# Optimization experiments

Hardware: AMD Instinct MI355X
Metric: run time of the kernel (lower is better)

Reference implementation:

```python
import jax, jax.numpy as jnp
import numpy as np

TEMPERATURE = 11.313708498984761  # sqrt(d_k) with d_k=128
RELU15_CAP = 15.0


def setup_inputs() -> dict:
    key = jax.random.key(0)
    kq, kk, kv = jax.random.split(key, 3)
    B, H, S, D = 4, 16, 1024, 128
    q = jax.random.normal(kq, (B, H, S, D), dtype=jnp.float32)
    k = jax.random.normal(kk, (B, H, S, D), dtype=jnp.float32)
    v = jax.random.normal(kv, (B, H, S, D), dtype=jnp.float32)
    mask = jnp.ones((B, 1, S, S), dtype=jnp.int32)  # broadcast over heads
    return {"q": q, "k": k, "v": v, "mask": mask}


def reference(q, k, v, mask):
    # attn = (q / temperature) @ k^T  -> [B,H,Sq,Sk]
    attn = jnp.einsum("bhqd,bhkd->bhqk", q / TEMPERATURE, k)
    # masked_fill(mask == 0, -1e9)
    attn = jnp.where(mask == 0, jnp.float32(-1e9), attn)
    # ReLU15 activation (custom softmax replacement): clamp to [0, 15]
    attn = jnp.clip(attn, 0.0, RELU15_CAP)
    # dropout with p=0.0 is identity (inference reference)
    out = jnp.einsum("bhqk,bhkd->bhqd", attn, v)
    return (out, attn)
```

## Files before the change

kernel.cpp:

```cpp
#include <hip/hip_runtime.h>
#include <stdint.h>

#define B_   4
#define H_   16
#define S_   1024
#define D_   128
#define BM   64
#define BN   32
#define NKT  (S_ / BN)
#define NTHREADS 256

typedef float f32x4 __attribute__((ext_vector_type(4)));
typedef short s16x8 __attribute__((ext_vector_type(8)));
typedef short s16x4 __attribute__((ext_vector_type(4)));

static __device__ __forceinline__ uint16_t f2bf(float f) {
  uint32_t u = __float_as_uint(f);
  u += 0x7FFFu + ((u >> 16) & 1u);
  return (uint16_t)(u >> 16);
}
static __device__ __forceinline__ float bf2f(uint16_t h) {
  return __uint_as_float((uint32_t)h << 16);
}

static __device__ __forceinline__ void gl16(const void* g, void* l) {
  __builtin_amdgcn_global_load_lds(
      (const __attribute__((address_space(1))) unsigned int*)g,
      (__attribute__((address_space(3))) unsigned int*)l, 16, 0, 0);
}

#define WSK_BYTES  16777216
#define WSV_BYTES  16777216
#define WSM_BYTES  524288
#define WS_NEED    (WSK_BYTES + WSV_BYTES + WSM_BYTES)

__global__ __launch_bounds__(256)
void prepass_kernel(const float* __restrict__ k, const float* __restrict__ v,
                    const int* __restrict__ mask,
                    char* __restrict__ wsK, char* __restrict__ wsV,
                    uint32_t* __restrict__ wsM)
{
  int gid = blockIdx.x * 256 + threadIdx.x;
  if (gid < 1048576) {
    int tile = gid >> 9, c = gid & 511;
    int ks = c >> 7, nt = (c >> 6) & 1, lane = c & 63;
    int row = (tile & 31) * 32 + 16 * nt + (lane & 15);
    int col = 32 * ks + 8 * (lane >> 4);
    const float* src = k + ((size_t)(tile >> 5) * S_ + row) * D_ + col;
    f32x4 x0 = *(const f32x4*)src;
    f32x4 x1 = *(const f32x4*)(src + 4);
    s16x8 h;
    h[0]=f2bf(x0[0]); h[1]=f2bf(x0[1]); h[2]=f2bf(x0[2]); h[3]=f2bf(x0[3]);
    h[4]=f2bf(x1[0]); h[5]=f2bf(x1[1]); h[6]=f2bf(x1[2]); h[7]=f2bf(x1[3]);
    *(s16x8*)(wsK + (size_t)gid * 16) = h;
  } else if (gid < 2097152) {
    int gv = gid - 1048576;
    int tile = gv >> 9, c = gv & 511;
    int nt = c >> 6, lane = c & 63;
    int d   = 16 * nt + (lane & 15);
    int kv0 = (tile & 31) * 32 + 8 * (lane >> 4);
    const float* src = v + ((size_t)(tile >> 5) * S_ + kv0) * D_ + d;
    s16x8 h;
    #pragma unroll
    for (int i = 0; i < 8; ++i) h[i] = f2bf(src[(size_t)i * D_]);
    *(s16x8*)(wsV + (size_t)gv * 16) = h;
  } else if (gid < 2228224) {
    int gm = gid - 2097152;
    const int* src = mask + (size_t)(gm >> 5) * S_ + (gm & 31) * 32;
    uint32_t bits = 0;
    #pragma unroll
    for (int i = 0; i < 32; ++i) bits |= (src[i] != 0 ? 1u : 0u) << i;
    wsM[gm] = bits;
  }
}

__global__ __launch_bounds__(NTHREADS)
__attribute__((amdgpu_waves_per_eu(4)))
void attn_relu15_main(const float* __restrict__ q,
                      const char* __restrict__ wsK, const char* __restrict__ wsV,
                      const uint32_t* __restrict__ wsM,
                      float* __restrict__ outp, float* __restrict__ attnp)
{
  const int blk = blockIdx.x;
  const int g   = (blk & 7) * 128 + (blk >> 3);
  const int bh  = g >> 4;
  const int qt  = g & 15;
  const int b   = bh >> 4;

  const int tid  = threadIdx.x;
  const int lane = tid & 63;
  const int wq   = tid >> 6;
  const int lhi  = lane >> 4;
  const int llo  = lane & 15;

  __shared__ __align__(16) char smem[36864];
  char* const lK0 = smem;
  char* const lV0 = smem + 16384;
  char* const lS  = smem + 32768 + wq * 1024;

  const float*    qg  = q + (size_t)bh * (S_ * D_) + (size_t)qt * BM * D_;
  const char*     kw  = wsK + (size_t)(bh * 32) * 8192;
  const char*     vw  = wsV + (size_t)(bh * 32) * 8192;
  const uint32_t* mw0 = wsM + (size_t)(b * 1024 + qt * BM + 16 * wq) * 32;
  float*          ag  = attnp + (size_t)bh * S_ * S_ + (size_t)qt * BM * S_;
  float*          og  = outp  + (size_t)bh * (S_ * D_) + (size_t)qt * BM * D_;

  const float invT = 0.08838834764831843f;

  s16x8 qf[4];
  {
    const float* qrow = qg + (size_t)(16 * wq + llo) * D_;
    #pragma unroll
    for (int ks = 0; ks < 4; ++ks) {
      int d0 = 32 * ks + 8 * lhi;
      f32x4 x0 = *(const f32x4*)(qrow + d0);
      f32x4 x1 = *(const f32x4*)(qrow + d0 + 4);
      s16x8 h;
      h[0]=f2bf(x0[0]*invT); h[1]=f2bf(x0[1]*invT); h[2]=f2bf(x0[2]*invT); h[3]=f2bf(x0[3]*invT);
      h[4]=f2bf(x1[0]*invT); h[5]=f2bf(x1[1]*invT); h[6]=f2bf(x1[2]*invT); h[7]=f2bf(x1[3]*invT);
      qf[ks] = h;
    }
  }

  #pragma unroll
  for (int rep = 0; rep < 2; ++rep) {
    gl16(kw + rep * 4096 + tid * 16, lK0 + rep * 4096 + wq * 1024);
    gl16(vw + rep * 4096 + tid * 16, lV0 + rep * 4096 + wq * 1024);
  }
  asm volatile("s_waitcnt vmcnt(0)" ::: "memory");
  __builtin_amdgcn_s_barrier();
  __builtin_amdgcn_sched_barrier(0);

  f32x4 oacc[8];
  #pragma unroll
  for (int i = 0; i < 8; ++i) oacc[i] = (f32x4){0.f,0.f,0.f,0.f};

  int cur = 0;
  for (int kt = 0; kt < NKT; ++kt) {
    const bool pf = (kt + 1 < NKT);
    char* lKc = lK0 + cur * 8192;
    char* lVc = lV0 + cur * 8192;

    uint32_t mwv[4];
    #pragma unroll
    for (int j = 0; j < 4; ++j)
      mwv[j] = mw0[(size_t)(4 * lhi + j) * 32 + kt];

    if (pf) {
      const char* kn = kw + (size_t)(kt + 1) * 8192;
      const char* vn = vw + (size_t)(kt + 1) * 8192;
      char* lKn = lK0 + (cur ^ 1) * 8192;
      char* lVn = lV0 + (cur ^ 1) * 8192;
      #pragma unroll
      for (int rep = 0; rep < 2; ++rep) {
        gl16(kn + rep * 4096 + tid * 16, lKn + rep * 4096 + wq * 1024);
        gl16(vn + rep * 4096 + tid * 16, lVn + rep * 4096 + wq * 1024);
      }
    }
    __builtin_amdgcn_sched_barrier(0);

    f32x4 sacc[2];
    sacc[0] = (f32x4){0.f,0.f,0.f,0.f}; sacc[1] = sacc[0];
    #pragma unroll
    for (int ks = 0; ks < 4; ++ks) {
      s16x8 bfr[2];
      #pragma unroll
      for (int nt = 0; nt < 2; ++nt)
        bfr[nt] = *(s16x8*)(lKc + (ks * 2 + nt) * 1024 + lane * 16);
      #pragma unroll
      for (int nt = 0; nt < 2; ++nt)
        sacc[nt] = __builtin_amdgcn_mfma_f32_16x16x32_bf16(qf[ks], bfr[nt], sacc[nt], 0, 0, 0);
    }

    #pragma unroll
    for (int nt = 0; nt < 2; ++nt) {
      char* sb = lS + (2 * nt + (llo >> 3)) * 256 + (llo & 7) * 2;
      #pragma unroll
      for (int j = 0; j < 4; ++j) {
        float val = fminf(fmaxf(sacc[nt][j], 0.f), 15.f);
        if (!((mwv[j] >> (16 * nt + llo)) & 1u)) val = 0.f;
        *(uint16_t*)(sb + (4 * lhi + j) * 16) = f2bf(val);
      }
    }

    {
      s16x8 saf = *(s16x8*)(lS + lane * 16);
      #pragma unroll
      for (int nt = 0; nt < 8; ++nt) {
        s16x8 vb = *(s16x8*)(lVc + nt * 1024 + lane * 16);
        oacc[nt] = __builtin_amdgcn_mfma_f32_16x16x32_bf16(saf, vb, oacc[nt], 0, 0, 0);
      }
    }

    #pragma unroll
    for (int p = 0; p < 2; ++p) {
      int r  = 16 * wq + p * 8 + (lane >> 3);
      int cb = lane & 7;
      s16x4 sv = *(s16x4*)(lS + (cb >> 1) * 256 + (((8 * p + (lane >> 3)) & 15) * 16) + (cb & 1) * 8);
      f32x4 a;
      a[0]=bf2f((uint16_t)sv[0]); a[1]=bf2f((uint16_t)sv[1]);
      a[2]=bf2f((uint16_t)sv[2]); a[3]=bf2f((uint16_t)sv[3]);
      __builtin_nontemporal_store(a, (f32x4*)(ag + (size_t)r * S_ + kt * BN + cb * 4));
    }

    asm volatile("s_waitcnt vmcnt(2)" ::: "memory");
    __builtin_amdgcn_s_barrier();
    __builtin_amdgcn_sched_barrier(0);
    cur ^= 1;
  }

  #pragma unroll
  for (int nt = 0; nt < 8; ++nt) {
    int n = 16 * nt + llo;
    #pragma unroll
    for (int j = 0; j < 4; ++j) {
      int m = 16 * wq + 4 * lhi + j;
      __builtin_nontemporal_store(oacc[nt][j], og + (size_t)m * D_ + n);
    }
  }
}

#define LDS_BARRIER() do {                                   \
    asm volatile("s_waitcnt lgkmcnt(0)" ::: "memory");       \
    __builtin_amdgcn_s_barrier();                            \
    __builtin_amdgcn_sched_barrier(0);                       \
  } while (0)

__global__ __launch_bounds__(NTHREADS)
__attribute__((amdgpu_waves_per_eu(4, 4)))
void attn_relu15_fallback(const float* __restrict__ q, const float* __restrict__ k,
                          const float* __restrict__ v, const int* __restrict__ mask,
                          float* __restrict__ outp, float* __restrict__ attnp)
{
  const int blk = blockIdx.x;
  const int g   = (blk & 7) * 128 + (blk >> 3);
  const int bh  = g >> 4;
  const int qt  = g & 15;
  const int b   = bh >> 4;
  const int tid  = threadIdx.x;
  const int lane = tid & 63;
  const int wq   = tid >> 6;
  const int lhi  = lane >> 4;
  const int llo  = lane & 15;

  __shared__ __align__(16) char smem[36864];
  char* const lK0 = smem;
  char* const lV0 = smem + 16384;
  char* const lS  = smem + 32768 + wq * 1024;

  const float* qg = q + (size_t)bh * (S_ * D_) + (size_t)qt * 64 * D_;
  const float* kg = k + (size_t)bh * (S_ * D_);
  const float* vg = v + (size_t)bh * (S_ * D_);
  const int*   mg = mask  + (size_t)b * S_ * S_ + (size_t)qt * 64 * S_;
  float*       ag = attnp + (size_t)bh * S_ * S_ + (size_t)qt * 64 * S_;
  float*       og = outp  + (size_t)bh * (S_ * D_) + (size_t)qt * 64 * D_;
  const float invT = 0.08838834764831843f;

  #define K_O(rep)   ((tid + NTHREADS * (rep)) * 8)
  #define K_ROW(o)   ((((o) >> 10) & 1) * 16 + (((o) >> 4) & 15))
  #define K_COL(o)   (((o) >> 11) * 32 + (((o) >> 8) & 3) * 8 + (((o) >> 3) & 1) * 4)

  s16x8 qf[4];
  {
    const float* qrow = qg + (size_t)(16 * wq + llo) * D_;
    #pragma unroll
    for (int ks = 0; ks < 4; ++ks) {
      int d0 = 32 * ks + 8 * lhi;
      f32x4 x0 = *(const f32x4*)(qrow + d0);
      f32x4 x1 = *(const f32x4*)(qrow + d0 + 4);
      s16x8 h;
      h[0]=f2bf(x0[0]*invT); h[1]=f2bf(x0[1]*invT); h[2]=f2bf(x0[2]*invT); h[3]=f2bf(x0[3]*invT);
      h[4]=f2bf(x1[0]*invT); h[5]=f2bf(x1[1]*invT); h[6]=f2bf(x1[2]*invT); h[7]=f2bf(x1[3]*invT);
      qf[ks] = h;
    }
  }
  {
    #pragma unroll
    for (int rep = 0; rep < 4; ++rep) {
      int o = K_O(rep);
      f32x4 x = *(const f32x4*)(kg + K_ROW(o) * D_ + K_COL(o));
      s16x4 h; h[0]=f2bf(x[0]); h[1]=f2bf(x[1]); h[2]=f2bf(x[2]); h[3]=f2bf(x[3]);
      *(s16x4*)(lK0 + o) = h;
    }
    #pragma unroll
    for (int rep = 0; rep < 4; ++rep) {
      int bid = (tid >> 2) + 64 * rep;
      int kb = bid >> 5, db = bid & 31, l2 = lane & 3;
      f32x4 x = *(const f32x4*)(vg + (size_t)(kb * 4 + l2) * D_ + db * 4);
      float v0=x[0], v1=x[1], v2=x[2], v3=x[3], t;
      t=(l2&1)?v0:v1; t=__shfl_xor(t,1); if(l2&1)v0=t; else v1=t;
      t=(l2&1)?v2:v3; t=__shfl_xor(t,1); if(l2&1)v2=t; else v3=t;
      t=(l2&2)?v0:v2; t=__shfl_xor(t,2); if(l2&2)v0=t; else v2=t;
      t=(l2&2)?v1:v3; t=__shfl_xor(t,2); if(l2&2)v1=t; else v3=t;
      int dd = db * 4 + l2;
      s16x4 h; h[0]=f2bf(v0); h[1]=f2bf(v1); h[2]=f2bf(v2); h[3]=f2bf(v3);
      *(s16x4*)(lV0 + (dd >> 4) * 1024 + ((kb >> 1) & 3) * 256
                    + (dd & 15) * 16 + (kb & 1) * 8) = h;
    }
  }
  LDS_BARRIER();

  f32x4 oacc[8];
  #pragma unroll
  for (int i = 0; i < 8; ++i) oacc[i] = (f32x4){0.f,0.f,0.f,0.f};

  int cur = 0;
  for (int kt = 0; kt < NKT; ++kt) {
    const bool pf = (kt + 1 < NKT);
    char* lKc = lK0 + cur * 8192;
    char* lVc = lV0 + cur * 8192;
    f32x4 kst[4];
    const float* kgt = kg + (size_t)(kt + 1) * BN * D_;
    if (pf) {
      #pragma unroll
      for (int rep = 0; rep < 4; ++rep) {
        int o = K_O(rep);
        kst[rep] = *(const f32x4*)(kgt + K_ROW(o) * D_ + K_COL(o));
      }
    }
    int mreg[8];
    #pragma unroll
    for (int nt = 0; nt < 2; ++nt)
      #pragma unroll
      for (int j = 0; j < 4; ++j)
        mreg[nt * 4 + j] =
          mg[(size_t)(16 * wq + 4 * lhi + j) * S_ + kt * BN + 16 * nt + llo];

    f32x4 sacc[2];
    sacc[0] = (f32x4){0.f,0.f,0.f,0.f}; sacc[1] = sacc[0];
    #pragma unroll
    for (int ks = 0; ks < 4; ++ks) {
      s16x8 bfr[2];
      #pragma unroll
      for (int nt = 0; nt < 2; ++nt)
        bfr[nt] = *(s16x8*)(lKc + (ks * 2 + nt) * 1024 + lane * 16);
      #pragma unroll
      for (int nt = 0; nt < 2; ++nt)
        sacc[nt] = __builtin_amdgcn_mfma_f32_16x16x32_bf16(qf[ks], bfr[nt], sacc[nt], 0, 0, 0);
    }

    f32x4 vst[4];
    const float* vgt = vg + (size_t)(kt + 1) * BN * D_;
    if (pf) {
      char* lKn = lK0 + (cur ^ 1) * 8192;
      #pragma unroll
      for (int rep = 0; rep < 4; ++rep) {
        f32x4 x = kst[rep];
        s16x4 h; h[0]=f2bf(x[0]); h[1]=f2bf(x[1]); h[2]=f2bf(x[2]); h[3]=f2bf(x[3]);
        *(s16x4*)(lKn + K_O(rep)) = h;
      }
      #pragma unroll
      for (int rep = 0; rep < 4; ++rep) {
        int bid = (tid >> 2) + 64 * rep;
        int kb = bid >> 5, db = bid & 31, l2 = lane & 3;
        vst[rep] = *(const f32x4*)(vgt + (size_t)(kb * 4 + l2) * D_ + db * 4);
      }
    }

    #pragma unroll
    for (int nt = 0; nt < 2; ++nt) {
      char* sb = lS + (2 * nt + (llo >> 3)) * 256 + (llo & 7) * 2;
      #pragma unroll
      for (int j = 0; j < 4; ++j) {
        float val = fminf(fmaxf(sacc[nt][j], 0.f), 15.f);
        if (mreg[nt * 4 + j] == 0) val = 0.f;
        *(uint16_t*)(sb + (4 * lhi + j) * 16) = f2bf(val);
      }
    }
    {
      s16x8 saf = *(s16x8*)(lS + lane * 16);
      #pragma unroll
      for (int nt = 0; nt < 8; ++nt) {
        s16x8 vb = *(s16x8*)(lVc + nt * 1024 + lane * 16);
        oacc[nt] = __builtin_amdgcn_mfma_f32_16x16x32_bf16(saf, vb, oacc[nt], 0, 0, 0);
      }
    }
    #pragma unroll
    for (int p = 0; p < 2; ++p) {
      int r  = 16 * wq + p * 8 + (lane >> 3);
      int cb = lane & 7;
      s16x4 sv = *(s16x4*)(lS + (cb >> 1) * 256 + ((r & 15) * 16) + (cb & 1) * 8);
      f32x4 a;
      a[0]=bf2f((uint16_t)sv[0]); a[1]=bf2f((uint16_t)sv[1]);
      a[2]=bf2f((uint16_t)sv[2]); a[3]=bf2f((uint16_t)sv[3]);
      __builtin_nontemporal_store(a, (f32x4*)(ag + (size_t)r * S_ + kt * BN + cb * 4));
    }
    if (pf) {
      char* lVn = lV0 + (cur ^ 1) * 8192;
      #pragma unroll
      for (int rep = 0; rep < 4; ++rep) {
        int bid = (tid >> 2) + 64 * rep;
        int kb = bid >> 5, db = bid & 31, l2 = lane & 3;
        f32x4 x = vst[rep];
        float v0=x[0], v1=x[1], v2=x[2], v3=x[3], t;
        t=(l2&1)?v0:v1; t=__shfl_xor(t,1); if(l2&1)v0=t; else v1=t;
        t=(l2&1)?v2:v3; t=__shfl_xor(t,1); if(l2&1)v2=t; else v3=t;
        t=(l2&2)?v0:v2; t=__shfl_xor(t,2); if(l2&2)v0=t; else v2=t;
        t=(l2&2)?v1:v3; t=__shfl_xor(t,2); if(l2&2)v1=t; else v3=t;
        int dd = db * 4 + l2;
        s16x4 h; h[0]=f2bf(v0); h[1]=f2bf(v1); h[2]=f2bf(v2); h[3]=f2bf(v3);
        *(s16x4*)(lVn + (dd >> 4) * 1024 + ((kb >> 1) & 3) * 256
                      + (dd & 15) * 16 + (kb & 1) * 8) = h;
      }
    }
    LDS_BARRIER();
    cur ^= 1;
  }
  #pragma unroll
  for (int nt = 0; nt < 8; ++nt) {
    int n = 16 * nt + llo;
    #pragma unroll
    for (int j = 0; j < 4; ++j) {
      int m = 16 * wq + 4 * lhi + j;
      __builtin_nontemporal_store(oacc[nt][j], og + (size_t)m * D_ + n);
    }
  }
}

extern "C" void kernel_launch(void* const* d_in, const int* in_sizes, int n_in,
                              void* d_out, int out_size, void* d_ws, size_t ws_size,
                              hipStream_t stream) {
  const float* q    = (const float*)d_in[0];
  const float* k    = (const float*)d_in[1];
  const float* v    = (const float*)d_in[2];
  const int*   mask = (const int*)d_in[3];
  float* outp  = (float*)d_out;
  float* attnp = outp + (size_t)B_ * H_ * S_ * D_;

  if (ws_size >= (size_t)WS_NEED && d_ws != nullptr) {
    char*     wsK = (char*)d_ws;
    char*     wsV = wsK + WSK_BYTES;
    uint32_t* wsM = (uint32_t*)(wsK + WSK_BYTES + WSV_BYTES);
    prepass_kernel<<<8704, 256, 0, stream>>>(k, v, mask, wsK, wsV, wsM);
    attn_relu15_main<<<dim3(B_ * H_ * (S_ / BM)), NTHREADS, 0, stream>>>(
        q, wsK, wsV, wsM, outp, attnp);
  } else {
    attn_relu15_fallback<<<dim3(B_ * H_ * (S_ / 64)), NTHREADS, 0, stream>>>(
        q, k, v, mask, outp, attnp);
  }
}
```

Before: 110.6 us.

## Switch main kernel to 32x32x16 MFMA with 128-row query tiles

```diff
diff --git a/kernel.cpp b/kernel.cpp
--- a/kernel.cpp
+++ b/kernel.cpp
@@ -5,14 +5,14 @@
 #define H_   16
 #define S_   1024
 #define D_   128
-#define BM   64
 #define BN   32
 #define NKT  (S_ / BN)
 #define NTHREADS 256
 
-typedef float f32x4 __attribute__((ext_vector_type(4)));
-typedef short s16x8 __attribute__((ext_vector_type(8)));
-typedef short s16x4 __attribute__((ext_vector_type(4)));
+typedef float f32x4  __attribute__((ext_vector_type(4)));
+typedef float f32x16 __attribute__((ext_vector_type(16)));
+typedef short s16x8  __attribute__((ext_vector_type(8)));
+typedef short s16x4  __attribute__((ext_vector_type(4)));
 
 static __device__ __forceinline__ uint16_t f2bf(float f) {
   uint32_t u = __float_as_uint(f);
@@ -43,10 +43,10 @@
   int gid = blockIdx.x * 256 + threadIdx.x;
   if (gid < 1048576) {
     int tile = gid >> 9, c = gid & 511;
-    int ks = c >> 7, nt = (c >> 6) & 1, lane = c & 63;
-    int row = (tile & 31) * 32 + 16 * nt + (lane & 15);
-    int col = 32 * ks + 8 * (lane >> 4);
-    const float* src = k + ((size_t)(tile >> 5) * S_ + row) * D_ + col;
+    int ks = c >> 6, l = c & 63;
+    int kv = l & 31, tt = l >> 5;
+    const float* src = k + ((size_t)(tile >> 5) * S_ + (tile & 31) * 32 + kv) * D_
+                         + 16 * ks + 8 * tt;
     f32x4 x0 = *(const f32x4*)src;
     f32x4 x1 = *(const f32x4*)(src + 4);
     s16x8 h;
@@ -56,13 +56,13 @@
   } else if (gid < 2097152) {
     int gv = gid - 1048576;
     int tile = gv >> 9, c = gv & 511;
-    int nt = c >> 6, lane = c & 63;
-    int d   = 16 * nt + (lane & 15);
-    int kv0 = (tile & 31) * 32 + 8 * (lane >> 4);
-    const float* src = v + ((size_t)(tile >> 5) * S_ + kv0) * D_ + d;
+    int l = c & 63;
+    int d   = 32 * (c >> 7) + (l & 31);
+    int kv0 = 16 * ((c >> 6) & 1) + 8 * (l >> 5);
+    const float* src = v + ((size_t)(tile >> 5) * S_ + (tile & 31) * 32 + kv0) * D_ + d;
     s16x8 h;
     #pragma unroll
-    for (int i = 0; i < 8; ++i) h[i] = f2bf(src[(size_t)i * D_]);
+    for (int e = 0; e < 8; ++e) h[e] = f2bf(src[(size_t)e * D_]);
     *(s16x8*)(wsV + (size_t)gv * 16) = h;
   } else if (gid < 2228224) {
     int gm = gid - 2097152;
@@ -75,46 +75,45 @@
 }
 
 __global__ __launch_bounds__(NTHREADS)
-__attribute__((amdgpu_waves_per_eu(4)))
+__attribute__((amdgpu_waves_per_eu(2)))
 void attn_relu15_main(const float* __restrict__ q,
                       const char* __restrict__ wsK, const char* __restrict__ wsV,
                       const uint32_t* __restrict__ wsM,
                       float* __restrict__ outp, float* __restrict__ attnp)
 {
   const int blk = blockIdx.x;
-  const int g   = (blk & 7) * 128 + (blk >> 3);
-  const int bh  = g >> 4;
-  const int qt  = g & 15;
+  const int g   = (blk & 7) * 64 + (blk >> 3);
+  const int bh  = g >> 3;
+  const int qt  = g & 7;
   const int b   = bh >> 4;
 
   const int tid  = threadIdx.x;
   const int lane = tid & 63;
-  const int wq   = tid >> 6;
-  const int lhi  = lane >> 4;
-  const int llo  = lane & 15;
-
-  __shared__ __align__(16) char smem[36864];
+  const int wv   = tid >> 6;
+  const int q31  = lane & 31;
+  const int t    = lane >> 5;
+  const int qrow0 = qt * 128 + wv * 32;
+
+  __shared__ __align__(16) char smem[41984];
   char* const lK0 = smem;
   char* const lV0 = smem + 16384;
-  char* const lS  = smem + 32768 + wq * 1024;
-
-  const float*    qg  = q + (size_t)bh * (S_ * D_) + (size_t)qt * BM * D_;
-  const char*     kw  = wsK + (size_t)(bh * 32) * 8192;
-  const char*     vw  = wsV + (size_t)(bh * 32) * 8192;
-  const uint32_t* mw0 = wsM + (size_t)(b * 1024 + qt * BM + 16 * wq) * 32;
-  float*          ag  = attnp + (size_t)bh * S_ * S_ + (size_t)qt * BM * S_;
-  float*          og  = outp  + (size_t)bh * (S_ * D_) + (size_t)qt * BM * D_;
+  char* const lS  = smem + 32768 + wv * 2304;
+
+  const char*     kw   = wsK + (size_t)(bh * 32) * 8192;
+  const char*     vw   = wsV + (size_t)(bh * 32) * 8192;
+  const uint32_t* mrow = wsM + (size_t)(b * 1024 + qrow0 + q31) * 32;
+  float*          ag   = attnp + ((size_t)bh * S_ + qrow0) * S_;
+  float*          og   = outp  + (size_t)bh * S_ * D_;
 
   const float invT = 0.08838834764831843f;
 
-  s16x8 qf[4];
+  s16x8 qf[8];
   {
-    const float* qrow = qg + (size_t)(16 * wq + llo) * D_;
-    #pragma unroll
-    for (int ks = 0; ks < 4; ++ks) {
-      int d0 = 32 * ks + 8 * lhi;
-      f32x4 x0 = *(const f32x4*)(qrow + d0);
-      f32x4 x1 = *(const f32x4*)(qrow + d0 + 4);
+    const float* qrow = q + ((size_t)bh * S_ + qrow0 + q31) * D_ + 8 * t;
+    #pragma unroll
+    for (int ks = 0; ks < 8; ++ks) {
+      f32x4 x0 = *(const f32x4*)(qrow + 16 * ks);
+      f32x4 x1 = *(const f32x4*)(qrow + 16 * ks + 4);
       s16x8 h;
       h[0]=f2bf(x0[0]*invT); h[1]=f2bf(x0[1]*invT); h[2]=f2bf(x0[2]*invT); h[3]=f2bf(x0[3]*invT);
       h[4]=f2bf(x1[0]*invT); h[5]=f2bf(x1[1]*invT); h[6]=f2bf(x1[2]*invT); h[7]=f2bf(x1[3]*invT);
@@ -124,16 +123,18 @@
 
   #pragma unroll
   for (int rep = 0; rep < 2; ++rep) {
-    gl16(kw + rep * 4096 + tid * 16, lK0 + rep * 4096 + wq * 1024);
-    gl16(vw + rep * 4096 + tid * 16, lV0 + rep * 4096 + wq * 1024);
-  }
-  asm volatile("s_waitcnt vmcnt(0)" ::: "memory");
+    gl16(kw + rep * 4096 + tid * 16, lK0 + rep * 4096 + wv * 1024);
+    gl16(vw + rep * 4096 + tid * 16, lV0 + rep * 4096 + wv * 1024);
+  }
+  asm volatile("s_waitcnt vmcnt(0) lgkmcnt(0)" ::: "memory");
   __builtin_amdgcn_s_barrier();
   __builtin_amdgcn_sched_barrier(0);
 
-  f32x4 oacc[8];
+  f32x16 oacc[4];
   #pragma unroll
-  for (int i = 0; i < 8; ++i) oacc[i] = (f32x4){0.f,0.f,0.f,0.f};
+  for (int dc = 0; dc < 4; ++dc)
+    #pragma unroll
+    for (int r = 0; r < 16; ++r) oacc[dc][r] = 0.f;
 
   int cur = 0;
   for (int kt = 0; kt < NKT; ++kt) {
@@ -141,10 +142,7 @@
     char* lKc = lK0 + cur * 8192;
     char* lVc = lV0 + cur * 8192;
 
-    uint32_t mwv[4];
-    #pragma unroll
-    for (int j = 0; j < 4; ++j)
-      mwv[j] = mw0[(size_t)(4 * lhi + j) * 32 + kt];
+    uint32_t mword = mrow[kt];
 
     if (pf) {
       const char* kn = kw + (size_t)(kt + 1) * 8192;
@@ -153,71 +151,70 @@
       char* lVn = lV0 + (cur ^ 1) * 8192;
       #pragma unroll
       for (int rep = 0; rep < 2; ++rep) {
-        gl16(kn + rep * 4096 + tid * 16, lKn + rep * 4096 + wq * 1024);
-        gl16(vn + rep * 4096 + tid * 16, lVn + rep * 4096 + wq * 1024);
+        gl16(kn + rep * 4096 + tid * 16, lKn + rep * 4096 + wv * 1024);
+        gl16(vn + rep * 4096 + tid * 16, lVn + rep * 4096 + wv * 1024);
       }
     }
     __builtin_amdgcn_sched_barrier(0);
 
-    f32x4 sacc[2];
-    sacc[0] = (f32x4){0.f,0.f,0.f,0.f}; sacc[1] = sacc[0];
-    #pragma unroll
-    for (int ks = 0; ks < 4; ++ks) {
-      s16x8 bfr[2];
-      #pragma unroll
-      for (int nt = 0; nt < 2; ++nt)
-        bfr[nt] = *(s16x8*)(lKc + (ks * 2 + nt) * 1024 + lane * 16);
-      #pragma unroll
-      for (int nt = 0; nt < 2; ++nt)
-        sacc[nt] = __builtin_amdgcn_mfma_f32_16x16x32_bf16(qf[ks], bfr[nt], sacc[nt], 0, 0, 0);
-    }
-
-    #pragma unroll
-    for (int nt = 0; nt < 2; ++nt) {
-      char* sb = lS + (2 * nt + (llo >> 3)) * 256 + (llo & 7) * 2;
+    f32x16 sacc;
+    #pragma unroll
+    for (int r = 0; r < 16; ++r) sacc[r] = 0.f;
+    #pragma unroll
+    for (int ks = 0; ks < 8; ++ks) {
+      s16x8 kf = *(s16x8*)(lKc + ks * 1024 + lane * 16);
+      sacc = __builtin_amdgcn_mfma_f32_32x32x16_bf16(kf, qf[ks], sacc, 0, 0, 0);
+    }
+
+    #pragma unroll
+    for (int gq = 0; gq < 4; ++gq) {
+      s16x4 h4;
       #pragma unroll
       for (int j = 0; j < 4; ++j) {
-        float val = fminf(fmaxf(sacc[nt][j], 0.f), 15.f);
-        if (!((mwv[j] >> (16 * nt + llo)) & 1u)) val = 0.f;
-        *(uint16_t*)(sb + (4 * lhi + j) * 16) = f2bf(val);
-      }
+        float val = fminf(fmaxf(sacc[4 * gq + j], 0.f), 15.f);
+        if (!((mword >> (8 * gq + 4 * t + j)) & 1u)) val = 0.f;
+        h4[j] = (short)f2bf(val);
+      }
+      *(s16x4*)(lS + q31 * 72 + 16 * gq + 8 * t) = h4;
     }
 
     {
-      s16x8 saf = *(s16x8*)(lS + lane * 16);
-      #pragma unroll
-      for (int nt = 0; nt < 8; ++nt) {
-        s16x8 vb = *(s16x8*)(lVc + nt * 1024 + lane * 16);
-        oacc[nt] = __builtin_amdgcn_mfma_f32_16x16x32_bf16(saf, vb, oacc[nt], 0, 0, 0);
-      }
-    }
-
-    #pragma unroll
-    for (int p = 0; p < 2; ++p) {
-      int r  = 16 * wq + p * 8 + (lane >> 3);
+      s16x8 saf0 = *(s16x8*)(lS + q31 * 72 + 16 * t);
+      s16x8 saf1 = *(s16x8*)(lS + q31 * 72 + 32 + 16 * t);
+      #pragma unroll
+      for (int dc = 0; dc < 4; ++dc) {
+        s16x8 vb0 = *(s16x8*)(lVc + (dc * 2 + 0) * 1024 + lane * 16);
+        oacc[dc] = __builtin_amdgcn_mfma_f32_32x32x16_bf16(saf0, vb0, oacc[dc], 0, 0, 0);
+        s16x8 vb1 = *(s16x8*)(lVc + (dc * 2 + 1) * 1024 + lane * 16);
+        oacc[dc] = __builtin_amdgcn_mfma_f32_32x32x16_bf16(saf1, vb1, oacc[dc], 0, 0, 0);
+      }
+    }
+
+    #pragma unroll
+    for (int p = 0; p < 4; ++p) {
+      int rr = 8 * p + (lane >> 3);
       int cb = lane & 7;
-      s16x4 sv = *(s16x4*)(lS + (cb >> 1) * 256 + (((8 * p + (lane >> 3)) & 15) * 16) + (cb & 1) * 8);
+      s16x4 sv = *(s16x4*)(lS + rr * 72 + cb * 8);
       f32x4 a;
       a[0]=bf2f((uint16_t)sv[0]); a[1]=bf2f((uint16_t)sv[1]);
       a[2]=bf2f((uint16_t)sv[2]); a[3]=bf2f((uint16_t)sv[3]);
-      __builtin_nontemporal_store(a, (f32x4*)(ag + (size_t)r * S_ + kt * BN + cb * 4));
-    }
-
-    asm volatile("s_waitcnt vmcnt(2)" ::: "memory");
+      __builtin_nontemporal_store(a,
+          (f32x4*)(ag + (size_t)rr * S_ + kt * BN + cb * 4));
+    }
+
+    asm volatile("s_waitcnt vmcnt(4) lgkmcnt(0)" ::: "memory");
     __builtin_amdgcn_s_barrier();
     __builtin_amdgcn_sched_barrier(0);
     cur ^= 1;
   }
 
   #pragma unroll
-  for (int nt = 0; nt < 8; ++nt) {
-    int n = 16 * nt + llo;
-    #pragma unroll
-    for (int j = 0; j < 4; ++j) {
-      int m = 16 * wq + 4 * lhi + j;
-      __builtin_nontemporal_store(oacc[nt][j], og + (size_t)m * D_ + n);
-    }
-  }
+  for (int dc = 0; dc < 4; ++dc)
+    #pragma unroll
+    for (int r = 0; r < 16; ++r) {
+      int row = qrow0 + (r & 3) + 8 * (r >> 2) + 4 * t;
+      __builtin_nontemporal_store(oacc[dc][r], og + (size_t)row * D_ + 32 * dc + q31);
+    }
 }
 
 #define LDS_BARRIER() do {                                   \
@@ -432,7 +429,7 @@
     char*     wsV = wsK + WSK_BYTES;
     uint32_t* wsM = (uint32_t*)(wsK + WSK_BYTES + WSV_BYTES);
     prepass_kernel<<<8704, 256, 0, stream>>>(k, v, mask, wsK, wsV, wsM);
-    attn_relu15_main<<<dim3(B_ * H_ * (S_ / BM)), NTHREADS, 0, stream>>>(
+    attn_relu15_main<<<dim3(512), NTHREADS, 0, stream>>>(
         q, wsK, wsV, wsM, outp, attnp);
   } else {
     attn_relu15_fallback<<<dim3(B_ * H_ * (S_ / 64)), NTHREADS, 0, stream>>>(
```

New measurement: 111.4 us. Within noise of the previous version (+0.7%).
